# Kernel tuning notes

Measured on AMD Instinct MI355X. Metric: run time of the kernel, lower is better.

Reference implementation:

```python
import jax, jax.numpy as jnp
import numpy as np

B, H, S, D = 1, 16, 2048, 128
SINK = 4            # SINK_LENGTH in source
QMAX = 7.0          # 4-bit symmetric: 2**(4-1)-1
K_OUT = 8           # outlier tokens kept per (b,h,d) channel slice (outlier_dim=-2)
V_OUT = 4           # outlier channels kept per (b,h,s) token slice (outlier_dim=-1)


def setup_inputs() -> dict:
    key = jax.random.key(0)
    kq, kk, kv = jax.random.split(key, 3)
    return {
        "q_tensor": jax.random.normal(kq, (B, H, S, D), jnp.float32),
        "k_tensor": jax.random.normal(kk, (B, H, S, D), jnp.float32),
        "v_tensor": jax.random.normal(kv, (B, H, S, D), jnp.float32),
    }


def _causal_attention(q, k, v):
    # standard SDPA, prefill chunk (cache empty), no RoPE (rotary_emb_module is None)
    scores = jnp.einsum("bhqd,bhkd->bhqk", q, k) * (D ** -0.5)
    causal = jnp.tril(jnp.ones((S, S), bool))
    scores = jnp.where(causal, scores, -1e30)
    probs = jax.nn.softmax(scores, axis=-1)
    return jnp.einsum("bhqk,bhkd->bhqd", probs, v)


def _isolate_k(x, n):
    # outlier_dim=-2: per (b,h,d) channel slice, pull top-n |.| tokens out as sparse
    xt = jnp.transpose(x, (0, 1, 3, 2))                     # [B,H,D,S]
    _, idx = jax.lax.top_k(jnp.abs(xt), n)                  # [B,H,D,n] token indices
    vals = jnp.take_along_axis(xt, idx, axis=-1)            # [B,H,D,n]
    bb = jnp.arange(B)[:, None, None, None]
    hh = jnp.arange(H)[None, :, None, None]
    dd = jnp.arange(D)[None, None, :, None]
    dense = jnp.transpose(xt.at[bb, hh, dd, idx].set(0.0), (0, 1, 3, 2))
    flat_idx = ((bb * H + hh) * S + idx) * D + dd           # flat index into [B,H,S,D]
    return dense, vals.reshape(-1), flat_idx.reshape(-1)


def _isolate_v(x, n):
    # outlier_dim=-1: per (b,h,s) token slice, pull top-n |.| channels out as sparse
    _, idx = jax.lax.top_k(jnp.abs(x), n)                   # [B,H,S,n] channel indices
    vals = jnp.take_along_axis(x, idx, axis=-1)
    bb = jnp.arange(B)[:, None, None, None]
    hh = jnp.arange(H)[None, :, None, None]
    ss = jnp.arange(S)[None, None, :, None]
    dense = x.at[bb, hh, ss, idx].set(0.0)
    flat_idx = ((bb * H + hh) * S + ss) * D + idx
    return dense, vals.reshape(-1), flat_idx.reshape(-1)


def _quantize_dense(x, absmax):
    scale = jnp.maximum(absmax, 1e-8) / QMAX
    q = jnp.clip(jnp.round(x / scale), -QMAX, QMAX)
    return q, scale


def reference(q_tensor, k_tensor, v_tensor):
    attn_output = _causal_attention(q_tensor, k_tensor, v_tensor)

    # chunk 0 prefill: zero sink tokens before outlier isolation
    k_iso = k_tensor.at[:, :, :SINK, :].set(0.0)
    v_iso = v_tensor.at[:, :, :SINK, :].set(0.0)

    k_dense, k_sp_val, k_sp_idx = _isolate_k(k_iso, K_OUT)
    v_dense, v_sp_val, v_sp_idx = _isolate_v(v_iso, V_OUT)

    # append full-precision sink tokens as sparse entries (flat indices)
    flat_ids = jnp.arange(B * H * S * D, dtype=jnp.int32).reshape(B, H, S, D)
    sink_idx = flat_ids[:, :, :SINK, :].reshape(-1)
    v_sp_val = jnp.concatenate([v_sp_val, v_tensor[:, :, :SINK, :].reshape(-1)])
    v_sp_idx = jnp.concatenate([v_sp_idx.astype(jnp.int32), sink_idx])
    k_sp_val = jnp.concatenate([k_sp_val, k_tensor[:, :, :SINK, :].reshape(-1)])
    k_sp_idx = jnp.concatenate([k_sp_idx.astype(jnp.int32), sink_idx])

    # key stats: per-channel absmax over tokens; value stats: per-token absmax over channels
    k_absmax = jnp.max(jnp.abs(k_dense), axis=2, keepdims=True)   # [B,H,1,D]
    v_absmax = jnp.max(jnp.abs(v_dense), axis=3, keepdims=True)   # [B,H,S,1]

    k_quant, k_scale = _quantize_dense(k_dense, k_absmax)
    v_quant, v_scale = _quantize_dense(v_dense, v_absmax)

    return (attn_output,
            k_quant, k_scale, k_sp_val, k_sp_idx,
            v_quant, v_scale, v_sp_val, v_sp_idx)
```

## Files before the change

kernel.cpp:

```cpp
#include <hip/hip_runtime.h>

#define HH 16
#define SS 2048
#define DD 128

#define O0 0u
#define O1 4194304u
#define O2 8388608u
#define O3 8390656u
#define O4 8415232u
#define O5 8439808u
#define O6 12634112u
#define O7 12666880u
#define O8 12806144u

using bf16x8 = __attribute__((ext_vector_type(8))) short;
using f32x4  = __attribute__((ext_vector_type(4))) float;

static __device__ __forceinline__ unsigned short f2bf(float f) {
  union { float f; unsigned u; } x; x.f = f;
  unsigned r = x.u + 0x7fffu + ((x.u >> 16) & 1u);
  return (unsigned short)(r >> 16);
}

static __device__ __forceinline__ unsigned pk2bf(float lo, float hi) {
  unsigned r;
  asm("v_cvt_pk_bf16_f32 %0, %1, %2" : "=v"(r) : "v"(lo), "v"(hi));
  return r;
}

typedef __attribute__((address_space(1))) const unsigned int gu32_t;
typedef __attribute__((address_space(3))) unsigned int lu32_t;
static __device__ __forceinline__ void gl_lds16(const void* g, void* l) {
  __builtin_amdgcn_global_load_lds((gu32_t*)g, (lu32_t*)l, 16, 0, 0);
}

#define INS9(a_, v_, i_)                                              \
  if ((a_) > aab[8]) {                                                \
    aab[8] = (a_); av[8] = (v_); ai[8] = (i_);                        \
    _Pragma("unroll")                                                 \
    for (int jj = 8; jj > 0; --jj) {                                  \
      if (aab[jj] > aab[jj - 1]) {                                    \
        float ta = aab[jj]; aab[jj] = aab[jj - 1]; aab[jj - 1] = ta;  \
        float tv = av[jj];  av[jj]  = av[jj - 1];  av[jj - 1]  = tv;  \
        int   ti = ai[jj];  ai[jj]  = ai[jj - 1];  ai[jj - 1]  = ti;  \
      }                                                               \
    }                                                                 \
  }

__global__ __launch_bounds__(256) void prep_kv(const float* __restrict__ K,
                                               const float* __restrict__ V,
                                               uint4* __restrict__ WK,
                                               uint4* __restrict__ WV,
                                               float* __restrict__ wval,
                                               int* __restrict__ widx) {
  __shared__ unsigned short T2u[128 * 72];
  const int bid = blockIdx.x;
  const int tid = threadIdx.x;

  if (bid < 256) {
    const int h  = bid >> 4;
    const int sb = bid & 15;
    const float* Kh = K + ((size_t)h * SS + (size_t)sb * 128) * DD;
    #pragma unroll
    for (int it = 0; it < 8; ++it) {
      const int idx = it * 256 + tid;
      const int tl  = idx >> 10;
      const int rem = idx & 1023;
      const int row = rem >> 4;
      const int c8  = rem & 15;
      const float* src = Kh + (size_t)(tl * 64 + row) * DD + c8 * 8;
      const float4 a = *(const float4*)src;
      const float4 b = *(const float4*)(src + 4);
      uint4 r;
      r.x = pk2bf(a.x, a.y);
      r.y = pk2bf(a.z, a.w);
      r.z = pk2bf(b.x, b.y);
      r.w = pk2bf(b.z, b.w);
      const int slot = ((row >> 4) * 4 + (c8 >> 2)) * 64 + (c8 & 3) * 16 + (row & 15);
      WK[(size_t)(h * 32 + sb * 2 + tl) * 1024 + slot] = r;
    }

  } else if (bid < 768) {
    const int ht = bid - 256;
    const float* Vh = V + (size_t)(ht >> 5) * (SS * DD) + (size_t)(ht & 31) * 64 * DD;

    #pragma unroll
    for (int it = 0; it < 4; ++it) {
      const int p   = it * 256 + tid;
      const int row = (p >> 5) * 2;
      const int col = (p & 31) * 4;
      const float4 a = *(const float4*)(Vh + (size_t)row * DD + col);
      const float4 b = *(const float4*)(Vh + (size_t)(row + 1) * DD + col);
      const float avv[4] = {a.x, a.y, a.z, a.w};
      const float bvv[4] = {b.x, b.y, b.z, b.w};
      #pragma unroll
      for (int jj = 0; jj < 4; ++jj) {
        const int n   = col + jj;
        const int swz = ((n >> 3) & 7) << 3;
        const int kk  = row ^ swz;
        *(unsigned*)&T2u[n * 72 + kk] = pk2bf(avv[jj], bvv[jj]);
      }
    }
    __syncthreads();

    uint4* dst = WV + (size_t)ht * 1024;
    #pragma unroll
    for (int it = 0; it < 4; ++it) {
      const int slot = it * 256 + tid;
      const int chunk = slot >> 6, l = slot & 63;
      const int c = chunk >> 1, tk = chunk & 1;
      const int n   = c * 16 + (l & 15);
      const int k0  = tk * 32 + (l >> 4) * 8;
      const int swz = ((n >> 3) & 7) << 3;
      dst[slot] = *(const uint4*)&T2u[n * 72 + (k0 ^ swz)];
    }

  } else {
    const int xb = bid - 768;
    const int h  = xb >> 4;
    const int sb = xb & 15;
    const float* Kh = K + (size_t)h * (SS * DD);
    const int d   = tid & 127;
    const int sub = tid >> 7;
    const int s0  = sb * 128 + sub * 64;

    float aab[9], av[9]; int ai[9];
    #pragma unroll
    for (int j = 0; j < 9; ++j) { aab[j] = -1.f; av[j] = 0.f; ai[j] = 0; }
    for (int ib = 0; ib < 64; ib += 8) {
      float vv[8];
      #pragma unroll
      for (int u = 0; u < 8; ++u)
        vv[u] = Kh[((size_t)(s0 + ib + u) << 7) + d];
      #pragma unroll
      for (int u = 0; u < 8; ++u) {
        const int s = s0 + ib + u;
        const float v = (s < 4) ? 0.f : vv[u];
        const float a = fabsf(v);
        INS9(a, v, s)
      }
    }
    float* lvf = (float*)T2u;
    int*   lii = (int*)T2u + 1152;
    if (sub == 1) {
      #pragma unroll
      for (int j = 0; j < 9; ++j) { lvf[d * 9 + j] = av[j]; lii[d * 9 + j] = ai[j]; }
    }
    __syncthreads();
    if (sub == 0) {
      #pragma unroll
      for (int j = 0; j < 9; ++j) {
        const float v = lvf[d * 9 + j];
        const int  s2 = lii[d * 9 + j];
        const float a = fabsf(v);
        INS9(a, v, s2)
      }
      const int base = (sb * 2048 + h * 128 + d) * 9;
      #pragma unroll
      for (int j = 0; j < 9; ++j) { wval[base + j] = av[j]; widx[base + j] = ai[j]; }
    }
  }
}

__global__ __launch_bounds__(256) void attn_ws(const float* __restrict__ Q,
                                               const uint4* __restrict__ WK,
                                               const uint4* __restrict__ WV,
                                               const float* __restrict__ wval,
                                               const int* __restrict__ widx,
                                               const float* __restrict__ K,
                                               const float* __restrict__ V,
                                               float* __restrict__ O) {
  const int bid = blockIdx.x;
  const int tid = threadIdx.x;

  if (bid < 8) {
    const int ch = bid * 256 + tid;
    const int h = ch >> 7, d = ch & 127;

    float aab[9], av[9]; int ai[9];
    #pragma unroll
    for (int j = 0; j < 9; ++j) { aab[j] = -1.f; av[j] = 0.f; ai[j] = 0; }

    float va[9], vb[9]; int ia[9], ib[9];
    {
      const int b0 = ch * 9;
      #pragma unroll
      for (int j = 0; j < 9; ++j) { va[j] = wval[b0 + j]; ia[j] = widx[b0 + j]; }
    }
    for (int sb = 0; sb < 16; ++sb) {
      if (sb < 15) {
        const int nb = ((sb + 1) * 2048 + ch) * 9;
        #pragma unroll
        for (int j = 0; j < 9; ++j) { vb[j] = wval[nb + j]; ib[j] = widx[nb + j]; }
      }
      #pragma unroll
      for (int j = 0; j < 9; ++j) {
        const float v = va[j];
        const int  si = ia[j];
        const float a = fabsf(v);
        INS9(a, v, si)
      }
      #pragma unroll
      for (int j = 0; j < 9; ++j) { va[j] = vb[j]; ia[j] = ib[j]; }
    }

    const float scale = fmaxf(aab[8], 1e-8f) / 7.0f;
    O[O2 + ch] = scale;
    #pragma unroll
    for (int j = 0; j < 8; ++j) {
      O[O3 + ch * 8u + j] = av[j];
      O[O4 + ch * 8u + j] = (float)((h * SS + ai[j]) * DD + d);
    }
    #pragma unroll
    for (int u = 0; u < 4; ++u) {
      const int i  = ch * 4 + u;
      const int hh = i >> 9;
      const int r  = i & 511;
      const int flat = hh * (SS * DD) + r;
      const float fidx = (float)flat;
      O[O3 + 16384u + i]  = K[flat];
      O[O4 + 16384u + i]  = fidx;
      O[O7 + 131072u + i] = V[flat];
      O[O8 + 131072u + i] = fidx;
    }
    return;
  }

  const int abid = bid - 8;
  const int x  = abid & 7;
  const int kk = abid >> 3;
  const int p_ = kk >> 5;
  const int r  = kk & 31;
  const int h  = x * 2 + (r & 1);
  const int jj = r >> 1;
  const int qb = p_ ? (31 - jj) : jj;
  const int q0 = qb << 6;
  const int w   = tid >> 6;
  const int l   = tid & 63;
  const int l15 = l & 15;
  const int lg  = l >> 4;

  __shared__ uint4 Kt[2][2048];
  __shared__ unsigned short Pl[4][16][72];

  bf16x8 qf[4];
  {
    const float* qp = Q + (size_t)h * (SS * DD) + (size_t)(q0 + w * 16 + l15) * DD + lg * 8;
    #pragma unroll
    for (int t = 0; t < 4; ++t) {
      const float4 a = *(const float4*)(qp + t * 32);
      const float4 b = *(const float4*)(qp + t * 32 + 4);
      bf16x8 f;
      f[0] = (short)f2bf(a.x); f[1] = (short)f2bf(a.y);
      f[2] = (short)f2bf(a.z); f[3] = (short)f2bf(a.w);
      f[4] = (short)f2bf(b.x); f[5] = (short)f2bf(b.y);
      f[6] = (short)f2bf(b.z); f[7] = (short)f2bf(b.w);
      qf[t] = f;
    }
  }

  f32x4 acc[8];
  #pragma unroll
  for (int c = 0; c < 8; ++c) acc[c] = (f32x4){0.f, 0.f, 0.f, 0.f};
  float lrow = 0.f;

  const float sc2 = 0.08838834764831845f * 1.4426950408889634f;

  {
    const size_t tbase = (size_t)(h * 32) * 1024;
    #pragma unroll
    for (int i = 0; i < 8; ++i) {
      const int ch = (w << 3) + i;
      gl_lds16(WK + tbase + ch * 64 + l, &Kt[0][ch * 64]);
    }
  }
  __syncthreads();

  const int npair = (qb >> 1) + 1;
  for (int it = 0; it < npair; ++it) {
    const int cur = it & 1;
    const int kt0 = it * 2;
    const bool has1 = (kt0 + 1 <= qb);

    uint4 vbr[16];
    {
      const uint4* gv = WV + (size_t)(h * 32 + kt0) * 1024 + l;
      #pragma unroll
      for (int c8 = 0; c8 < 16; ++c8) vbr[c8] = gv[c8 * 64];
    }

    if (it + 1 < npair) {
      const size_t tbase = (size_t)(h * 32 + kt0 + 2) * 1024;
      #pragma unroll
      for (int i = 0; i < 8; ++i) {
        const int ch = (w << 3) + i;
        gl_lds16(WK + tbase + ch * 64 + l, &Kt[cur ^ 1][ch * 64]);
      }
    }

    {
      const bool diag = (kt0 == qb);
      const int ctmax = diag ? (w + 1) : 4;
      float p[4][4];
      __builtin_amdgcn_s_setprio(1);
      #pragma unroll
      for (int ct = 0; ct < 4; ++ct) {
        if (ct < ctmax) {
          f32x4 a = (f32x4){0.f, 0.f, 0.f, 0.f};
          #pragma unroll
          for (int t = 0; t < 4; ++t) {
            bf16x8 kb = ((const bf16x8*)Kt[cur])[(ct * 4 + t) * 64 + l];
            a = __builtin_amdgcn_mfma_f32_16x16x32_bf16(kb, qf[t], a, 0, 0, 0);
          }
          #pragma unroll
          for (int r2 = 0; r2 < 4; ++r2) {
            float s = a[r2] * sc2;
            if (diag) {
              const int koff = ct * 16 + lg * 4 + r2;
              s = (koff > w * 16 + l15) ? -1e30f : s;
            }
            p[ct][r2] = s;
          }
        }
      }
      __builtin_amdgcn_s_setprio(0);

      #pragma unroll
      for (int ct = 0; ct < 4; ++ct) {
        if (ct < ctmax) {
          #pragma unroll
          for (int r2 = 0; r2 < 4; ++r2) {
            const float e = exp2f(p[ct][r2]);
            p[ct][r2] = e;
            lrow += e;
          }
        } else {
          #pragma unroll
          for (int r2 = 0; r2 < 4; ++r2) p[ct][r2] = 0.f;
        }
      }

      #pragma unroll
      for (int ct = 0; ct < 4; ++ct) {
        uint2 pk;
        pk.x = (unsigned)f2bf(p[ct][0]) | ((unsigned)f2bf(p[ct][1]) << 16);
        pk.y = (unsigned)f2bf(p[ct][2]) | ((unsigned)f2bf(p[ct][3]) << 16);
        *(uint2*)&Pl[w][l15][ct * 16 + lg * 4] = pk;
      }

      __builtin_amdgcn_s_setprio(1);
      #pragma unroll
      for (int tk = 0; tk < 2; ++tk) {
        bf16x8 pa = *(const bf16x8*)&Pl[w][l15][tk * 32 + lg * 8];
        #pragma unroll
        for (int c = 0; c < 8; ++c) {
          bf16x8 vb = *(const bf16x8*)&vbr[c * 2 + tk];
          acc[c] = __builtin_amdgcn_mfma_f32_16x16x32_bf16(pa, vb, acc[c], 0, 0, 0);
        }
      }
      __builtin_amdgcn_s_setprio(0);
    }

    if (has1) {
      const int kt1 = kt0 + 1;
      {
        const uint4* gv = WV + (size_t)(h * 32 + kt1) * 1024 + l;
        #pragma unroll
        for (int c8 = 0; c8 < 16; ++c8) vbr[c8] = gv[c8 * 64];
      }
      const bool diag = (kt1 == qb);
      const int ctmax = diag ? (w + 1) : 4;
      float p[4][4];
      __builtin_amdgcn_s_setprio(1);
      #pragma unroll
      for (int ct = 0; ct < 4; ++ct) {
        if (ct < ctmax) {
          f32x4 a = (f32x4){0.f, 0.f, 0.f, 0.f};
          #pragma unroll
          for (int t = 0; t < 4; ++t) {
            bf16x8 kb = ((const bf16x8*)Kt[cur])[(16 + ct * 4 + t) * 64 + l];
            a = __builtin_amdgcn_mfma_f32_16x16x32_bf16(kb, qf[t], a, 0, 0, 0);
          }
          #pragma unroll
          for (int r2 = 0; r2 < 4; ++r2) {
            float s = a[r2] * sc2;
            if (diag) {
              const int koff = ct * 16 + lg * 4 + r2;
              s = (koff > w * 16 + l15) ? -1e30f : s;
            }
            p[ct][r2] = s;
          }
        }
      }
      __builtin_amdgcn_s_setprio(0);

      #pragma unroll
      for (int ct = 0; ct < 4; ++ct) {
        if (ct < ctmax) {
          #pragma unroll
          for (int r2 = 0; r2 < 4; ++r2) {
            const float e = exp2f(p[ct][r2]);
            p[ct][r2] = e;
            lrow += e;
          }
        } else {
          #pragma unroll
          for (int r2 = 0; r2 < 4; ++r2) p[ct][r2] = 0.f;
        }
      }

      #pragma unroll
      for (int ct = 0; ct < 4; ++ct) {
        uint2 pk;
        pk.x = (unsigned)f2bf(p[ct][0]) | ((unsigned)f2bf(p[ct][1]) << 16);
        pk.y = (unsigned)f2bf(p[ct][2]) | ((unsigned)f2bf(p[ct][3]) << 16);
        *(uint2*)&Pl[w][l15][ct * 16 + lg * 4] = pk;
      }

      __builtin_amdgcn_s_setprio(1);
      #pragma unroll
      for (int tk = 0; tk < 2; ++tk) {
        bf16x8 pa = *(const bf16x8*)&Pl[w][l15][tk * 32 + lg * 8];
        #pragma unroll
        for (int c = 0; c < 8; ++c) {
          bf16x8 vb = *(const bf16x8*)&vbr[c * 2 + tk];
          acc[c] = __builtin_amdgcn_mfma_f32_16x16x32_bf16(pa, vb, acc[c], 0, 0, 0);
        }
      }
      __builtin_amdgcn_s_setprio(0);
    }

    __syncthreads();
  }

  lrow += __shfl_xor(lrow, 16);
  lrow += __shfl_xor(lrow, 32);
  const float inv = 1.0f / lrow;
  float invr[4];
  #pragma unroll
  for (int r2 = 0; r2 < 4; ++r2) invr[r2] = __shfl(inv, lg * 4 + r2);
  #pragma unroll
  for (int r2 = 0; r2 < 4; ++r2) {
    const int row = q0 + w * 16 + lg * 4 + r2;
    float* op = O + O0 + (size_t)(h * SS + row) * DD;
    #pragma unroll
    for (int c = 0; c < 8; ++c)
      op[c * 16 + l15] = acc[c][r2] * invr[r2];
  }
}

__global__ __launch_bounds__(256) void attn_fb(const float* __restrict__ Q,
                                               const float* __restrict__ K,
                                               const float* __restrict__ V,
                                               float* __restrict__ O) {
  const int h   = blockIdx.x >> 5;
  const int q0  = (blockIdx.x & 31) << 6;
  const int tid = threadIdx.x;
  const int w   = tid >> 6;
  const int l   = tid & 63;
  const int l15 = l & 15;
  const int lg  = l >> 4;

  __shared__ unsigned short Kl[64][136];
  __shared__ unsigned short Vt[128][72];
  __shared__ unsigned short Pl[4][16][72];

  const size_t hbase = (size_t)h * (SS * DD);
  const float* Qh = Q + hbase;
  const float* Kh = K + hbase;
  const float* Vh = V + hbase;

  bf16x8 qf[4];
  {
    const float* qp = Qh + (size_t)(q0 + w * 16 + l15) * DD + lg * 8;
    #pragma unroll
    for (int t = 0; t < 4; ++t) {
      bf16x8 f;
      #pragma unroll
      for (int j = 0; j < 8; ++j) f[j] = (short)f2bf(qp[t * 32 + j]);
      qf[t] = f;
    }
  }

  f32x4 acc[8];
  #pragma unroll
  for (int c = 0; c < 8; ++c) acc[c] = (f32x4){0.f, 0.f, 0.f, 0.f};
  float mrow[4], lrow[4];
  #pragma unroll
  for (int r = 0; r < 4; ++r) { mrow[r] = -1e30f; lrow[r] = 0.f; }

  const float sc2 = 0.08838834764831845f * 1.4426950408889634f;

  const int ntile = (q0 >> 6) + 1;
  for (int kt = 0; kt < ntile; ++kt) {
    const int kv0 = kt << 6;
    __syncthreads();
    for (int idx = tid; idx < 64 * 128; idx += 256) {
      const int kv = idx >> 7, d = idx & 127;
      const size_t g = (size_t)(kv0 + kv) * DD + d;
      Kl[kv][d] = f2bf(Kh[g]);
      Vt[d][kv] = f2bf(Vh[g]);
    }
    __syncthreads();

    f32x4 sacc[4];
    #pragma unroll
    for (int ct = 0; ct < 4; ++ct) {
      f32x4 a = (f32x4){0.f, 0.f, 0.f, 0.f};
      #pragma unroll
      for (int t = 0; t < 4; ++t) {
        bf16x8 kb = *(const bf16x8*)&Kl[ct * 16 + l15][t * 32 + lg * 8];
        a = __builtin_amdgcn_mfma_f32_16x16x32_bf16(qf[t], kb, a, 0, 0, 0);
      }
      sacc[ct] = a;
    }

    float sv[4][4];
    #pragma unroll
    for (int ct = 0; ct < 4; ++ct) {
      const int col = kv0 + ct * 16 + l15;
      #pragma unroll
      for (int r = 0; r < 4; ++r) {
        const int row = q0 + w * 16 + lg * 4 + r;
        sv[ct][r] = (col > row) ? -1e30f : sacc[ct][r] * sc2;
      }
    }

    #pragma unroll
    for (int r = 0; r < 4; ++r) {
      float mt = fmaxf(fmaxf(sv[0][r], sv[1][r]), fmaxf(sv[2][r], sv[3][r]));
      #pragma unroll
      for (int m = 1; m < 16; m <<= 1) mt = fmaxf(mt, __shfl_xor(mt, m));
      const float mn = fmaxf(mrow[r], mt);
      const float al = exp2f(mrow[r] - mn);
      mrow[r] = mn;
      float rs = 0.f;
      #pragma unroll
      for (int ct = 0; ct < 4; ++ct) {
        const float p = exp2f(sv[ct][r] - mn);
        sv[ct][r] = p;
        rs += p;
      }
      #pragma unroll
      for (int m = 1; m < 16; m <<= 1) rs += __shfl_xor(rs, m);
      lrow[r] = lrow[r] * al + rs;
      #pragma unroll
      for (int c = 0; c < 8; ++c) acc[c][r] *= al;
    }

    #pragma unroll
    for (int ct = 0; ct < 4; ++ct)
      #pragma unroll
      for (int r = 0; r < 4; ++r)
        Pl[w][lg * 4 + r][ct * 16 + l15] = f2bf(sv[ct][r]);

    #pragma unroll
    for (int tk = 0; tk < 2; ++tk) {
      bf16x8 pa = *(const bf16x8*)&Pl[w][l15][tk * 32 + lg * 8];
      #pragma unroll
      for (int c = 0; c < 8; ++c) {
        bf16x8 vb = *(const bf16x8*)&Vt[c * 16 + l15][tk * 32 + lg * 8];
        acc[c] = __builtin_amdgcn_mfma_f32_16x16x32_bf16(pa, vb, acc[c], 0, 0, 0);
      }
    }
  }

  #pragma unroll
  for (int r = 0; r < 4; ++r) {
    const float inv = 1.0f / lrow[r];
    const int row = q0 + w * 16 + lg * 4 + r;
    float* op = O + O0 + (size_t)(h * SS + row) * DD;
    #pragma unroll
    for (int c = 0; c < 8; ++c)
      op[c * 16 + l15] = acc[c][r] * inv;
  }
}

__global__ __launch_bounds__(256) void v_kernel(const float* __restrict__ V,
                                                float* __restrict__ out) {
  const int gw = (blockIdx.x << 2) + (threadIdx.x >> 6);
  const int l  = threadIdx.x & 63;
  const int s  = gw & (SS - 1);
  const float2 v2 = ((const float2*)(V + (size_t)gw * DD))[l];
  const bool sink = (s < 4);
  const float w0 = sink ? 0.f : v2.x;
  const float w1 = sink ? 0.f : v2.y;
  float a0 = fabsf(w0), a1 = fabsf(w1);
  const int d0 = 2 * l, d1 = 2 * l + 1;

  float oval[4]; int oidx[4]; float scale = 0.f;
  #pragma unroll
  for (int rnd = 0; rnd < 5; ++rnd) {
    float ba; int bd; float bv;
    if (a1 > a0) { ba = a1; bd = d1; bv = w1; }
    else         { ba = a0; bd = d0; bv = w0; }
    #pragma unroll
    for (int m = 1; m < 64; m <<= 1) {
      const float oa = __shfl_xor(ba, m);
      const int   od = __shfl_xor(bd, m);
      const float ov = __shfl_xor(bv, m);
      if (oa > ba || (oa == ba && od < bd)) { ba = oa; bd = od; bv = ov; }
    }
    if (rnd < 4) {
      oval[rnd] = bv; oidx[rnd] = bd;
      if (bd == d0) a0 = -1.f;
      if (bd == d1) a1 = -1.f;
    } else {
      scale = fmaxf(ba, 1e-8f) / 7.0f;
    }
  }

  const bool z0 = (oidx[0] == d0) | (oidx[1] == d0) | (oidx[2] == d0) | (oidx[3] == d0);
  const bool z1 = (oidx[0] == d1) | (oidx[1] == d1) | (oidx[2] == d1) | (oidx[3] == d1);
  const float q0 = z0 ? 0.f : fminf(7.f, fmaxf(-7.f, rintf(w0 / scale)));
  const float q1 = z1 ? 0.f : fminf(7.f, fmaxf(-7.f, rintf(w1 / scale)));
  float2 pack; pack.x = q0; pack.y = q1;
  *(float2*)(out + O5 + (size_t)gw * DD + d0) = pack;

  if (l == 0) {
    out[O6 + gw] = scale;
    #pragma unroll
    for (int j = 0; j < 4; ++j) {
      out[O7 + gw * 4 + j] = oval[j];
      out[O8 + gw * 4 + j] = (float)(gw * DD + oidx[j]);
    }
  }
}

__global__ __launch_bounds__(256) void k_top(const float* __restrict__ K,
                                             float* __restrict__ out) {
  const int h  = blockIdx.x;
  const int t  = threadIdx.x;
  const int st = t >> 7;
  const float* Kh = K + (size_t)h * (SS * DD);

  __shared__ float lv[256][9];
  __shared__ int   li[256][9];

  float aab[9], av[9]; int ai[9];
  #pragma unroll
  for (int j = 0; j < 9; ++j) { aab[j] = -1.f; av[j] = 0.f; ai[j] = 0; }

  const int d = t & 127;
  const int s0 = st << 10;
  for (int i = 0; i < 1024; ++i) {
    const int s = s0 + i;
    float v = Kh[((size_t)s << 7) + d];
    if (s < 4) v = 0.f;
    const float a = fabsf(v);
    INS9(a, v, s)
  }

  #pragma unroll
  for (int j = 0; j < 9; ++j) { lv[t][j] = av[j]; li[t][j] = ai[j]; }
  __syncthreads();

  if (t < 128) {
    #pragma unroll
    for (int j = 0; j < 9; ++j) {
      const float v = lv[t + 128][j];
      const int  s2 = li[t + 128][j];
      const float a = fabsf(v);
      INS9(a, v, s2)
    }
    const float scale = fmaxf(aab[8], 1e-8f) / 7.0f;
    const unsigned ch = (unsigned)(h * 128 + t);
    out[O2 + ch] = scale;
    #pragma unroll
    for (int j = 0; j < 8; ++j) {
      out[O3 + ch * 8u + j] = av[j];
      out[O4 + ch * 8u + j] = (float)((h * SS + ai[j]) * DD + t);
    }
  }
}

__global__ __launch_bounds__(256) void sink_kernel(const float* __restrict__ K,
                                                   const float* __restrict__ V,
                                                   float* __restrict__ out) {
  const int i = blockIdx.x * 256 + threadIdx.x;
  const int h = i >> 9;
  const int r = i & 511;
  const int flat = h * (SS * DD) + r;
  const float fidx = (float)flat;
  out[O3 + 16384u + i]  = K[flat];
  out[O4 + 16384u + i]  = fidx;
  out[O7 + 131072u + i] = V[flat];
  out[O8 + 131072u + i] = fidx;
}

__global__ __launch_bounds__(256) void k_quant(const float* __restrict__ K,
                                               const float* __restrict__ V,
                                               const float* __restrict__ outr,
                                               float* __restrict__ out) {
  const int bid = blockIdx.x;
  const int tid = threadIdx.x;

  if (bid >= 4096) {
    const int gw = ((bid - 4096) << 2) + (tid >> 6);
    const int l  = tid & 63;
    const int s  = gw & (SS - 1);
    const float2 v2 = ((const float2*)(V + (size_t)gw * DD))[l];
    const bool sink = (s < 4);
    const float w0 = sink ? 0.f : v2.x;
    const float w1 = sink ? 0.f : v2.y;
    float a0 = fabsf(w0), a1 = fabsf(w1);
    const int d0 = 2 * l, d1 = 2 * l + 1;

    float oval[4]; int oidx[4]; float scale = 0.f;
    #pragma unroll
    for (int rnd = 0; rnd < 5; ++rnd) {
      float ba; int bd; float bv;
      if (a1 > a0) { ba = a1; bd = d1; bv = w1; }
      else         { ba = a0; bd = d0; bv = w0; }
      #pragma unroll
      for (int m = 1; m < 64; m <<= 1) {
        const float oa = __shfl_xor(ba, m);
        const int   od = __shfl_xor(bd, m);
        const float ov = __shfl_xor(bv, m);
        if (oa > ba || (oa == ba && od < bd)) { ba = oa; bd = od; bv = ov; }
      }
      if (rnd < 4) {
        oval[rnd] = bv; oidx[rnd] = bd;
        if (bd == d0) a0 = -1.f;
        if (bd == d1) a1 = -1.f;
      } else {
        scale = fmaxf(ba, 1e-8f) / 7.0f;
      }
    }

    const bool z0 = (oidx[0] == d0) | (oidx[1] == d0) | (oidx[2] == d0) | (oidx[3] == d0);
    const bool z1 = (oidx[0] == d1) | (oidx[1] == d1) | (oidx[2] == d1) | (oidx[3] == d1);
    const float q0 = z0 ? 0.f : fminf(7.f, fmaxf(-7.f, rintf(w0 / scale)));
    const float q1 = z1 ? 0.f : fminf(7.f, fmaxf(-7.f, rintf(w1 / scale)));
    float2 pack; pack.x = q0; pack.y = q1;
    *(float2*)(out + O5 + (size_t)gw * DD + d0) = pack;

    if (l == 0) {
      out[O6 + gw] = scale;
      #pragma unroll
      for (int j = 0; j < 4; ++j) {
        out[O7 + gw * 4 + j] = oval[j];
        out[O8 + gw * 4 + j] = (float)(gw * DD + oidx[j]);
      }
    }
    return;
  }

  __shared__ float ssc[128];
  __shared__ int   sid[128][8];
  const int e0 = bid * 1024;
  const int h  = e0 >> 18;
  if (tid < 128) {
    const unsigned ch = (unsigned)(h * 128 + tid);
    ssc[tid] = outr[O2 + ch];
    #pragma unroll
    for (int j = 0; j < 8; ++j)
      sid[tid][j] = ((int)outr[O4 + ch * 8u + j] >> 7) & (SS - 1);
  }
  __syncthreads();

  const int e  = e0 + tid * 4;
  const int dd = e & 127;
  const int s  = (e >> 7) & (SS - 1);
  const float4 kv = *(const float4*)(K + e);
  const float vv[4] = {kv.x, kv.y, kv.z, kv.w};
  float4 res;
  float rr[4];
  #pragma unroll
  for (int jj = 0; jj < 4; ++jj) {
    const int d = dd + jj;
    bool zero = (s < 4);
    #pragma unroll
    for (int j = 0; j < 8; ++j) zero |= (sid[d][j] == s);
    rr[jj] = zero ? 0.f : fminf(7.f, fmaxf(-7.f, rintf(vv[jj] / ssc[d])));
  }
  res.x = rr[0]; res.y = rr[1]; res.z = rr[2]; res.w = rr[3];
  *(float4*)(out + O1 + e) = res;
}

extern "C" void kernel_launch(void* const* d_in, const int* in_sizes, int n_in,
                              void* d_out, int out_size, void* d_ws, size_t ws_size,
                              hipStream_t stream) {
  const float* q = (const float*)d_in[0];
  const float* k = (const float*)d_in[1];
  const float* v = (const float*)d_in[2];
  float* out = (float*)d_out;

  const size_t nBF   = 524288;
  const size_t nPart = (size_t)2048 * 16 * 9;
  const size_t needFull = nBF * 2 * sizeof(uint4) + nPart * 8;

  uint4* wsk = (uint4*)d_ws;
  uint4* wsv = wsk + nBF;
  float* wval = (float*)(wsv + nBF);
  int*   widx = (int*)(wval + nPart);

  if (ws_size >= needFull) {
    prep_kv<<<dim3(1024), dim3(256), 0, stream>>>(k, v, wsk, wsv, wval, widx);
    attn_ws<<<dim3(520), dim3(256), 0, stream>>>(q, wsk, wsv, wval, widx, k, v, out);
    k_quant<<<dim3(4096 + HH * SS / 4), dim3(256), 0, stream>>>(k, v, out, out);
  } else {
    attn_fb<<<dim3(512), dim3(256), 0, stream>>>(q, k, v, out);
    v_kernel<<<dim3(HH * SS / 4), dim3(256), 0, stream>>>(v, out);
    k_top<<<dim3(HH), dim3(256), 0, stream>>>(k, out);
    sink_kernel<<<dim3(32), dim3(256), 0, stream>>>(k, v, out);
    k_quant<<<dim3(4096), dim3(256), 0, stream>>>(k, v, out, out);
  }
}
```

Baseline: 168.9 us.

## Move V outlier/quant into prep kernel and split K/V bf16 prep blocks finer

Moves the per-token V top-4 outlier extraction and quantization out of the final k_quant launch and into prep_kv, so it runs before attention and no longer extends the tail kernel. The K and V bf16 repacking work is split into smaller blocks (64 tokens per K block, half-width V tiles) with a smaller shared buffer, which doubles the number of blocks for better load spread and occupancy. In exchange, prep_kv grows much larger and sits in front of attention on the critical path.

```diff
diff --git a/kernel.cpp b/kernel.cpp
--- a/kernel.cpp
+++ b/kernel.cpp
@@ -53,23 +53,22 @@
                                                uint4* __restrict__ WK,
                                                uint4* __restrict__ WV,
                                                float* __restrict__ wval,
-                                               int* __restrict__ widx) {
-  __shared__ unsigned short T2u[128 * 72];
+                                               int* __restrict__ widx,
+                                               float* __restrict__ out) {
+  __shared__ unsigned short T2u[64 * 72];
   const int bid = blockIdx.x;
   const int tid = threadIdx.x;
 
-  if (bid < 256) {
-    const int h  = bid >> 4;
-    const int sb = bid & 15;
-    const float* Kh = K + ((size_t)h * SS + (size_t)sb * 128) * DD;
-    #pragma unroll
-    for (int it = 0; it < 8; ++it) {
+  if (bid < 512) {
+    const int h   = bid >> 5;
+    const int kvt = bid & 31;
+    const float* Kh = K + ((size_t)h * SS + (size_t)kvt * 64) * DD;
+    #pragma unroll
+    for (int it = 0; it < 4; ++it) {
       const int idx = it * 256 + tid;
-      const int tl  = idx >> 10;
-      const int rem = idx & 1023;
-      const int row = rem >> 4;
-      const int c8  = rem & 15;
-      const float* src = Kh + (size_t)(tl * 64 + row) * DD + c8 * 8;
+      const int row = idx >> 4;
+      const int c8  = idx & 15;
+      const float* src = Kh + (size_t)row * DD + c8 * 8;
       const float4 a = *(const float4*)src;
       const float4 b = *(const float4*)(src + 4);
       uint4 r;
@@ -78,18 +77,21 @@
       r.z = pk2bf(b.x, b.y);
       r.w = pk2bf(b.z, b.w);
       const int slot = ((row >> 4) * 4 + (c8 >> 2)) * 64 + (c8 & 3) * 16 + (row & 15);
-      WK[(size_t)(h * 32 + sb * 2 + tl) * 1024 + slot] = r;
-    }
-
-  } else if (bid < 768) {
-    const int ht = bid - 256;
+      WK[(size_t)(h * 32 + kvt) * 1024 + slot] = r;
+    }
+
+  } else if (bid < 1536) {
+    const int vb   = bid - 512;
+    const int ht   = vb >> 1;
+    const int half = vb & 1;
+    const int n0   = half * 64;
     const float* Vh = V + (size_t)(ht >> 5) * (SS * DD) + (size_t)(ht & 31) * 64 * DD;
 
     #pragma unroll
-    for (int it = 0; it < 4; ++it) {
-      const int p   = it * 256 + tid;
-      const int row = (p >> 5) * 2;
-      const int col = (p & 31) * 4;
+    for (int it = 0; it < 2; ++it) {
+      const int p    = it * 256 + tid;
+      const int row  = (p >> 4) * 2;
+      const int col  = n0 + (p & 15) * 4;
       const float4 a = *(const float4*)(Vh + (size_t)row * DD + col);
       const float4 b = *(const float4*)(Vh + (size_t)(row + 1) * DD + col);
       const float avv[4] = {a.x, a.y, a.z, a.w};
@@ -99,25 +101,28 @@
         const int n   = col + jj;
         const int swz = ((n >> 3) & 7) << 3;
         const int kk  = row ^ swz;
-        *(unsigned*)&T2u[n * 72 + kk] = pk2bf(avv[jj], bvv[jj]);
+        *(unsigned*)&T2u[(n - n0) * 72 + kk] = pk2bf(avv[jj], bvv[jj]);
       }
     }
     __syncthreads();
 
     uint4* dst = WV + (size_t)ht * 1024;
     #pragma unroll
-    for (int it = 0; it < 4; ++it) {
-      const int slot = it * 256 + tid;
-      const int chunk = slot >> 6, l = slot & 63;
-      const int c = chunk >> 1, tk = chunk & 1;
-      const int n   = c * 16 + (l & 15);
-      const int k0  = tk * 32 + (l >> 4) * 8;
-      const int swz = ((n >> 3) & 7) << 3;
-      dst[slot] = *(const uint4*)&T2u[n * 72 + (k0 ^ swz)];
-    }
-
-  } else {
-    const int xb = bid - 768;
+    for (int it = 0; it < 2; ++it) {
+      const int s2   = it * 256 + tid;
+      const int ch8  = s2 >> 6;
+      const int l    = s2 & 63;
+      const int c    = half * 4 + (ch8 >> 1);
+      const int tk   = ch8 & 1;
+      const int chunk = c * 2 + tk;
+      const int n    = c * 16 + (l & 15);
+      const int k0   = tk * 32 + (l >> 4) * 8;
+      const int swz  = ((n >> 3) & 7) << 3;
+      dst[chunk * 64 + l] = *(const uint4*)&T2u[(n - n0) * 72 + (k0 ^ swz)];
+    }
+
+  } else if (bid < 1792) {
+    const int xb = bid - 1536;
     const int h  = xb >> 4;
     const int sb = xb & 15;
     const float* Kh = K + (size_t)h * (SS * DD);
@@ -159,6 +164,55 @@
       const int base = (sb * 2048 + h * 128 + d) * 9;
       #pragma unroll
       for (int j = 0; j < 9; ++j) { wval[base + j] = av[j]; widx[base + j] = ai[j]; }
+    }
+
+  } else {
+    const int gw = ((bid - 1792) << 2) + (tid >> 6);
+    const int l  = tid & 63;
+    const int s  = gw & (SS - 1);
+    const float2 v2 = ((const float2*)(V + (size_t)gw * DD))[l];
+    const bool sink = (s < 4);
+    const float w0 = sink ? 0.f : v2.x;
+    const float w1 = sink ? 0.f : v2.y;
+    float a0 = fabsf(w0), a1 = fabsf(w1);
+    const int d0 = 2 * l, d1 = 2 * l + 1;
+
+    float oval[4]; int oidx[4]; float scale = 0.f;
+    #pragma unroll
+    for (int rnd = 0; rnd < 5; ++rnd) {
+      float ba; int bd; float bv;
+      if (a1 > a0) { ba = a1; bd = d1; bv = w1; }
+      else         { ba = a0; bd = d0; bv = w0; }
+      #pragma unroll
+      for (int m = 1; m < 64; m <<= 1) {
+        const float oa = __shfl_xor(ba, m);
+        const int   od = __shfl_xor(bd, m);
+        const float ov = __shfl_xor(bv, m);
+        if (oa > ba || (oa == ba && od < bd)) { ba = oa; bd = od; bv = ov; }
+      }
+      if (rnd < 4) {
+        oval[rnd] = bv; oidx[rnd] = bd;
+        if (bd == d0) a0 = -1.f;
+        if (bd == d1) a1 = -1.f;
+      } else {
+        scale = fmaxf(ba, 1e-8f) / 7.0f;
+      }
+    }
+
+    const bool z0 = (oidx[0] == d0) | (oidx[1] == d0) | (oidx[2] == d0) | (oidx[3] == d0);
+    const bool z1 = (oidx[0] == d1) | (oidx[1] == d1) | (oidx[2] == d1) | (oidx[3] == d1);
+    const float q0 = z0 ? 0.f : fminf(7.f, fmaxf(-7.f, rintf(w0 / scale)));
+    const float q1 = z1 ? 0.f : fminf(7.f, fmaxf(-7.f, rintf(w1 / scale)));
+    float2 pack; pack.x = q0; pack.y = q1;
+    *(float2*)(out + O5 + (size_t)gw * DD + d0) = pack;
+
+    if (l == 0) {
+      out[O6 + gw] = scale;
+      #pragma unroll
+      for (int j = 0; j < 4; ++j) {
+        out[O7 + gw * 4 + j] = oval[j];
+        out[O8 + gw * 4 + j] = (float)(gw * DD + oidx[j]);
+      }
     }
   }
 }
@@ -690,77 +744,22 @@
 }
 
 __global__ __launch_bounds__(256) void k_quant(const float* __restrict__ K,
-                                               const float* __restrict__ V,
                                                const float* __restrict__ outr,
                                                float* __restrict__ out) {
-  const int bid = blockIdx.x;
-  const int tid = threadIdx.x;
-
-  if (bid >= 4096) {
-    const int gw = ((bid - 4096) << 2) + (tid >> 6);
-    const int l  = tid & 63;
-    const int s  = gw & (SS - 1);
-    const float2 v2 = ((const float2*)(V + (size_t)gw * DD))[l];
-    const bool sink = (s < 4);
-    const float w0 = sink ? 0.f : v2.x;
-    const float w1 = sink ? 0.f : v2.y;
-    float a0 = fabsf(w0), a1 = fabsf(w1);
-    const int d0 = 2 * l, d1 = 2 * l + 1;
-
-    float oval[4]; int oidx[4]; float scale = 0.f;
-    #pragma unroll
-    for (int rnd = 0; rnd < 5; ++rnd) {
-      float ba; int bd; float bv;
-      if (a1 > a0) { ba = a1; bd = d1; bv = w1; }
-      else         { ba = a0; bd = d0; bv = w0; }
-      #pragma unroll
-      for (int m = 1; m < 64; m <<= 1) {
-        const float oa = __shfl_xor(ba, m);
-        const int   od = __shfl_xor(bd, m);
-        const float ov = __shfl_xor(bv, m);
-        if (oa > ba || (oa == ba && od < bd)) { ba = oa; bd = od; bv = ov; }
-      }
-      if (rnd < 4) {
-        oval[rnd] = bv; oidx[rnd] = bd;
-        if (bd == d0) a0 = -1.f;
-        if (bd == d1) a1 = -1.f;
-      } else {
-        scale = fmaxf(ba, 1e-8f) / 7.0f;
-      }
-    }
-
-    const bool z0 = (oidx[0] == d0) | (oidx[1] == d0) | (oidx[2] == d0) | (oidx[3] == d0);
-    const bool z1 = (oidx[0] == d1) | (oidx[1] == d1) | (oidx[2] == d1) | (oidx[3] == d1);
-    const float q0 = z0 ? 0.f : fminf(7.f, fmaxf(-7.f, rintf(w0 / scale)));
-    const float q1 = z1 ? 0.f : fminf(7.f, fmaxf(-7.f, rintf(w1 / scale)));
-    float2 pack; pack.x = q0; pack.y = q1;
-    *(float2*)(out + O5 + (size_t)gw * DD + d0) = pack;
-
-    if (l == 0) {
-      out[O6 + gw] = scale;
-      #pragma unroll
-      for (int j = 0; j < 4; ++j) {
-        out[O7 + gw * 4 + j] = oval[j];
-        out[O8 + gw * 4 + j] = (float)(gw * DD + oidx[j]);
-      }
-    }
-    return;
-  }
-
   __shared__ float ssc[128];
   __shared__ int   sid[128][8];
-  const int e0 = bid * 1024;
+  const int e0 = blockIdx.x * 1024;
   const int h  = e0 >> 18;
-  if (tid < 128) {
-    const unsigned ch = (unsigned)(h * 128 + tid);
-    ssc[tid] = outr[O2 + ch];
+  if (threadIdx.x < 128) {
+    const unsigned ch = (unsigned)(h * 128 + threadIdx.x);
+    ssc[threadIdx.x] = outr[O2 + ch];
     #pragma unroll
     for (int j = 0; j < 8; ++j)
-      sid[tid][j] = ((int)outr[O4 + ch * 8u + j] >> 7) & (SS - 1);
+      sid[threadIdx.x][j] = ((int)outr[O4 + ch * 8u + j] >> 7) & (SS - 1);
   }
   __syncthreads();
 
-  const int e  = e0 + tid * 4;
+  const int e  = e0 + threadIdx.x * 4;
   const int dd = e & 127;
   const int s  = (e >> 7) & (SS - 1);
   const float4 kv = *(const float4*)(K + e);
@@ -797,14 +796,14 @@
   int*   widx = (int*)(wval + nPart);
 
   if (ws_size >= needFull) {
-    prep_kv<<<dim3(1024), dim3(256), 0, stream>>>(k, v, wsk, wsv, wval, widx);
+    prep_kv<<<dim3(1792 + HH * SS / 4), dim3(256), 0, stream>>>(k, v, wsk, wsv, wval, widx, out);
     attn_ws<<<dim3(520), dim3(256), 0, stream>>>(q, wsk, wsv, wval, widx, k, v, out);
-    k_quant<<<dim3(4096 + HH * SS / 4), dim3(256), 0, stream>>>(k, v, out, out);
+    k_quant<<<dim3(4096), dim3(256), 0, stream>>>(k, out, out);
   } else {
     attn_fb<<<dim3(512), dim3(256), 0, stream>>>(q, k, v, out);
     v_kernel<<<dim3(HH * SS / 4), dim3(256), 0, stream>>>(v, out);
     k_top<<<dim3(HH), dim3(256), 0, stream>>>(k, out);
     sink_kernel<<<dim3(32), dim3(256), 0, stream>>>(k, v, out);
-    k_quant<<<dim3(4096), dim3(256), 0, stream>>>(k, v, out, out);
-  }
-}
+    k_quant<<<dim3(4096), dim3(256), 0, stream>>>(k, out, out);
+  }
+}
```

New measurement: 198.3 us. 1.17x slower.
